# Kernel optimization log

Measured on AMD Instinct MI355X. Metric: run time of the kernel, lower is better.

Reference implementation:

```python
import jax, jax.numpy as jnp
import numpy as np

B, N = 64, 1024


def setup_inputs() -> dict:
    key = jax.random.key(0)
    k1, k2, k3, k4 = jax.random.split(key, 4)
    successor_logits = jax.random.normal(k1, (B, N, N), dtype=jnp.float32)
    predecessor_logits = jax.random.normal(k2, (B, N, N), dtype=jnp.float32)
    # labels in [-1, N); -1 means 'points to self'
    successor_labels = jax.random.randint(k3, (B, N), -1, N, dtype=jnp.int64)
    predecessor_labels = jax.random.randint(k4, (B, N), -1, N, dtype=jnp.int64)
    line_mask = jnp.ones((B, N), dtype=bool)
    return {
        "successor_logits": successor_logits,
        "successor_labels": successor_labels,
        "predecessor_logits": predecessor_logits,
        "predecessor_labels": predecessor_labels,
        "line_mask": line_mask,
        "pred_weight": jnp.float32(1.0),
    }


def _direction_loss(logits, labels, line_mask, is_self_pointing):
    b, n = labels.shape
    line_idx = jnp.arange(n)
    # relabel self-pointing lines to their own index
    labels_fixed = jnp.where(is_self_pointing, line_idx[None, :], labels)
    # overwrite diagonal logit with (row max + 1) where self-pointing & valid
    row_max = jnp.max(logits, axis=-1)  # [B, N]
    cond = is_self_pointing & line_mask  # [B, N]
    eye = jnp.eye(n, dtype=bool)
    logits_adj = jnp.where(cond[:, :, None] & eye[None], (row_max + 1.0)[:, :, None], logits)
    # softmax cross-entropy per line
    logp = jax.nn.log_softmax(logits_adj, axis=-1)  # [B, N, N]
    lbl = jnp.clip(labels_fixed, 0, n - 1)
    nll = -jnp.take_along_axis(logp, lbl[:, :, None], axis=-1)[..., 0]  # [B, N]
    valid = line_mask.astype(logits.dtype)
    denom = jnp.maximum(valid.sum(), 1.0)
    return (nll * valid).sum() / denom


def reference(successor_logits, successor_labels, predecessor_logits,
              predecessor_labels, line_mask, pred_weight):
    last_line_mask = successor_labels == -1
    succ_loss = _direction_loss(successor_logits, successor_labels, line_mask, last_line_mask)
    first_line_mask = predecessor_labels == -1
    pred_loss = _direction_loss(predecessor_logits, predecessor_labels, line_mask, first_line_mask)
    total_loss = succ_loss + pred_weight * pred_loss
    num_valid = line_mask.sum()
    return total_loss, succ_loss, pred_loss, num_valid
```

## Files before the change

kernel.cpp:

```cpp
#include <hip/hip_runtime.h>
#include <math.h>

#define N_ 1024
#define ROWS_PER_DIR 65536
#define TOTAL_ROWS   131072
#define BLOCKS_K1    32768

__global__ __launch_bounds__(256) void row_loss_kernel(
    const float* __restrict__ succ_logits,
    const int*   __restrict__ succ_labels,
    const float* __restrict__ pred_logits,
    const int*   __restrict__ pred_labels,
    const int*   __restrict__ line_mask,
    float*       __restrict__ partials)
{
    __shared__ float wsum[4];
    const int wave = threadIdx.x >> 6;
    const int lane = threadIdx.x & 63;
    const int r    = blockIdx.x * 4 + wave;
    const int dir  = r >> 16;
    const int rr   = r & (ROWS_PER_DIR - 1);
    const int n    = rr & (N_ - 1);

    const float* __restrict__ logits = dir ? pred_logits : succ_logits;
    const int*   __restrict__ labels = dir ? pred_labels : succ_labels;
    const float* __restrict__ row    = logits + (size_t)rr * N_;

    const float4* row4 = (const float4*)row;
    float4 v0 = row4[0 * 64 + lane];
    float4 v1 = row4[1 * 64 + lane];
    float4 v2 = row4[2 * 64 + lane];
    float4 v3 = row4[3 * 64 + lane];

    float m = v0.x;
    m = fmaxf(m, v0.y); m = fmaxf(m, v0.z); m = fmaxf(m, v0.w);
    m = fmaxf(m, v1.x); m = fmaxf(m, v1.y); m = fmaxf(m, v1.z); m = fmaxf(m, v1.w);
    m = fmaxf(m, v2.x); m = fmaxf(m, v2.y); m = fmaxf(m, v2.z); m = fmaxf(m, v2.w);
    m = fmaxf(m, v3.x); m = fmaxf(m, v3.y); m = fmaxf(m, v3.z); m = fmaxf(m, v3.w);

    float s = 0.0f;
    s += __expf(v0.x - m); s += __expf(v0.y - m); s += __expf(v0.z - m); s += __expf(v0.w - m);
    s += __expf(v1.x - m); s += __expf(v1.y - m); s += __expf(v1.z - m); s += __expf(v1.w - m);
    s += __expf(v2.x - m); s += __expf(v2.y - m); s += __expf(v2.z - m); s += __expf(v2.w - m);
    s += __expf(v3.x - m); s += __expf(v3.y - m); s += __expf(v3.z - m); s += __expf(v3.w - m);

    #pragma unroll
    for (int off = 32; off > 0; off >>= 1) {
        float mo = __shfl_xor(m, off);
        float so = __shfl_xor(s, off);
        float M  = fmaxf(m, mo);
        s = s * __expf(m - M) + so * __expf(mo - M);
        m = M;
    }

    if (lane == 0) {
        float nll_masked = 0.0f;
        const int label = labels[rr];
        const int valid = line_mask[rr];
        if (valid) {
            if (label == -1) {
                float d = row[n];
                float s_adj = (s - __expf(d - m)) * 0.36787944117144233f + 1.0f;
                nll_masked = __logf(s_adj);
            } else {
                int lbl = label < 0 ? 0 : (label > N_ - 1 ? N_ - 1 : label);
                nll_masked = m + __logf(s) - row[lbl];
            }
        }
        wsum[wave] = nll_masked;
    }
    __syncthreads();
    if (threadIdx.x == 0)
        partials[blockIdx.x] = (wsum[0] + wsum[1]) + (wsum[2] + wsum[3]);
}

__global__ __launch_bounds__(1024) void finalize_kernel(
    const float* __restrict__ partials,
    const int*   __restrict__ line_mask,
    const float* __restrict__ pred_weight,
    float*       __restrict__ out)
{
    const int tid = threadIdx.x;
    float ssum = 0.0f, psum = 0.0f, msum = 0.0f;
    for (int i = tid; i < BLOCKS_K1 / 2; i += 1024) {
        ssum += partials[i];
        psum += partials[i + BLOCKS_K1 / 2];
    }
    for (int i = tid; i < ROWS_PER_DIR; i += 1024)
        msum += (line_mask[i] != 0) ? 1.0f : 0.0f;

    #pragma unroll
    for (int off = 32; off > 0; off >>= 1) {
        ssum += __shfl_xor(ssum, off);
        psum += __shfl_xor(psum, off);
        msum += __shfl_xor(msum, off);
    }

    __shared__ float sh[3][16];
    const int wave = tid >> 6, lane = tid & 63;
    if (lane == 0) { sh[0][wave] = ssum; sh[1][wave] = psum; sh[2][wave] = msum; }
    __syncthreads();
    if (tid == 0) {
        float S = 0.0f, P = 0.0f, M = 0.0f;
        #pragma unroll
        for (int w = 0; w < 16; ++w) { S += sh[0][w]; P += sh[1][w]; M += sh[2][w]; }
        const float denom = fmaxf(M, 1.0f);
        const float sl = S / denom, pl = P / denom;
        const float w  = pred_weight[0];
        out[0] = sl + w * pl;
        out[1] = sl;
        out[2] = pl;
        out[3] = M;
    }
}

extern "C" void kernel_launch(void* const* d_in, const int* in_sizes, int n_in,
                              void* d_out, int out_size, void* d_ws, size_t ws_size,
                              hipStream_t stream) {
    const float* succ_logits = (const float*)d_in[0];
    const int*   succ_labels = (const int*)  d_in[1];
    const float* pred_logits = (const float*)d_in[2];
    const int*   pred_labels = (const int*)  d_in[3];
    const int*   line_mask   = (const int*)  d_in[4];
    const float* pred_weight = (const float*)d_in[5];
    float* out      = (float*)d_out;
    float* partials = (float*)d_ws;

    row_loss_kernel<<<BLOCKS_K1, 256, 0, stream>>>(
        succ_logits, succ_labels, pred_logits, pred_labels, line_mask, partials);
    finalize_kernel<<<1, 1024, 0, stream>>>(partials, line_mask, pred_weight, out);
}
```

Before: 523.9 us.

## Use nontemporal loads, two-pass wave reduction, and in-register target gather

Reads rows with nontemporal vector loads and raises the block to 8 waves. The max reduction now finishes across the wave before the exp pass, so the cross-lane sum reduction no longer needs rescaling exps. The target logit is taken from registers with a shuffle instead of a second global load, and label and mask are loaded early. The kernel is bound by memory bandwidth, so the main lever is how the streaming reads are cached. The shuffle-based gather adds a little ALU work.

```diff
diff --git a/kernel.cpp b/kernel.cpp
--- a/kernel.cpp
+++ b/kernel.cpp
@@ -4,9 +4,12 @@
 #define N_ 1024
 #define ROWS_PER_DIR 65536
 #define TOTAL_ROWS   131072
-#define BLOCKS_K1    32768
+#define WAVES_PER_BLOCK 8
+#define BLOCKS_K1    (TOTAL_ROWS / WAVES_PER_BLOCK)
 
-__global__ __launch_bounds__(256) void row_loss_kernel(
+typedef float v4f __attribute__((ext_vector_type(4)));
+
+__global__ __launch_bounds__(512) void row_loss_kernel(
     const float* __restrict__ succ_logits,
     const int*   __restrict__ succ_labels,
     const float* __restrict__ pred_logits,
@@ -14,10 +17,10 @@
     const int*   __restrict__ line_mask,
     float*       __restrict__ partials)
 {
-    __shared__ float wsum[4];
+    __shared__ float wsum[WAVES_PER_BLOCK];
     const int wave = threadIdx.x >> 6;
     const int lane = threadIdx.x & 63;
-    const int r    = blockIdx.x * 4 + wave;
+    const int r    = blockIdx.x * WAVES_PER_BLOCK + wave;
     const int dir  = r >> 16;
     const int rr   = r & (ROWS_PER_DIR - 1);
     const int n    = rr & (N_ - 1);
@@ -26,52 +29,62 @@
     const int*   __restrict__ labels = dir ? pred_labels : succ_labels;
     const float* __restrict__ row    = logits + (size_t)rr * N_;
 
-    const float4* row4 = (const float4*)row;
-    float4 v0 = row4[0 * 64 + lane];
-    float4 v1 = row4[1 * 64 + lane];
-    float4 v2 = row4[2 * 64 + lane];
-    float4 v3 = row4[3 * 64 + lane];
+    const int label = labels[rr];
+    const int valid = line_mask[rr];
 
-    float m = v0.x;
-    m = fmaxf(m, v0.y); m = fmaxf(m, v0.z); m = fmaxf(m, v0.w);
-    m = fmaxf(m, v1.x); m = fmaxf(m, v1.y); m = fmaxf(m, v1.z); m = fmaxf(m, v1.w);
-    m = fmaxf(m, v2.x); m = fmaxf(m, v2.y); m = fmaxf(m, v2.z); m = fmaxf(m, v2.w);
-    m = fmaxf(m, v3.x); m = fmaxf(m, v3.y); m = fmaxf(m, v3.z); m = fmaxf(m, v3.w);
+    const v4f* row4 = (const v4f*)row;
+    v4f v0 = __builtin_nontemporal_load(row4 + 0 * 64 + lane);
+    v4f v1 = __builtin_nontemporal_load(row4 + 1 * 64 + lane);
+    v4f v2 = __builtin_nontemporal_load(row4 + 2 * 64 + lane);
+    v4f v3 = __builtin_nontemporal_load(row4 + 3 * 64 + lane);
+
+    const int t      = (label == -1) ? n : (label < 0 ? 0 : (label > N_ - 1 ? N_ - 1 : label));
+    const int t_lane = (t >> 2) & 63;
+    const int t_k    = t >> 8;
+    const int t_c    = t & 3;
+    v4f tv = (t_k == 0) ? v0 : (t_k == 1) ? v1 : (t_k == 2) ? v2 : v3;
+    const float x_t = __shfl(tv[t_c], t_lane);
+
+    float m;
+    {
+        v4f a = v0, b = v1;
+        a.x = fmaxf(a.x, b.x); a.y = fmaxf(a.y, b.y); a.z = fmaxf(a.z, b.z); a.w = fmaxf(a.w, b.w);
+        v4f c = v2; b = v3;
+        c.x = fmaxf(c.x, b.x); c.y = fmaxf(c.y, b.y); c.z = fmaxf(c.z, b.z); c.w = fmaxf(c.w, b.w);
+        a.x = fmaxf(a.x, c.x); a.y = fmaxf(a.y, c.y); a.z = fmaxf(a.z, c.z); a.w = fmaxf(a.w, c.w);
+        m = fmaxf(fmaxf(a.x, a.y), fmaxf(a.z, a.w));
+    }
+    #pragma unroll
+    for (int off = 32; off > 0; off >>= 1)
+        m = fmaxf(m, __shfl_xor(m, off));
 
     float s = 0.0f;
     s += __expf(v0.x - m); s += __expf(v0.y - m); s += __expf(v0.z - m); s += __expf(v0.w - m);
     s += __expf(v1.x - m); s += __expf(v1.y - m); s += __expf(v1.z - m); s += __expf(v1.w - m);
     s += __expf(v2.x - m); s += __expf(v2.y - m); s += __expf(v2.z - m); s += __expf(v2.w - m);
     s += __expf(v3.x - m); s += __expf(v3.y - m); s += __expf(v3.z - m); s += __expf(v3.w - m);
-
     #pragma unroll
-    for (int off = 32; off > 0; off >>= 1) {
-        float mo = __shfl_xor(m, off);
-        float so = __shfl_xor(s, off);
-        float M  = fmaxf(m, mo);
-        s = s * __expf(m - M) + so * __expf(mo - M);
-        m = M;
-    }
+    for (int off = 32; off > 0; off >>= 1)
+        s += __shfl_xor(s, off);
 
     if (lane == 0) {
-        float nll_masked = 0.0f;
-        const int label = labels[rr];
-        const int valid = line_mask[rr];
+        float nll = 0.0f;
         if (valid) {
             if (label == -1) {
-                float d = row[n];
-                float s_adj = (s - __expf(d - m)) * 0.36787944117144233f + 1.0f;
-                nll_masked = __logf(s_adj);
+                nll = __logf((s - __expf(x_t - m)) * 0.36787944117144233f + 1.0f);
             } else {
-                int lbl = label < 0 ? 0 : (label > N_ - 1 ? N_ - 1 : label);
-                nll_masked = m + __logf(s) - row[lbl];
+                nll = m + __logf(s) - x_t;
             }
         }
-        wsum[wave] = nll_masked;
+        wsum[wave] = nll;
     }
     __syncthreads();
-    if (threadIdx.x == 0)
-        partials[blockIdx.x] = (wsum[0] + wsum[1]) + (wsum[2] + wsum[3]);
+    if (threadIdx.x == 0) {
+        float acc = 0.0f;
+        #pragma unroll
+        for (int w = 0; w < WAVES_PER_BLOCK; ++w) acc += wsum[w];
+        partials[blockIdx.x] = acc;
+    }
 }
 
 __global__ __launch_bounds__(1024) void finalize_kernel(
@@ -126,7 +139,7 @@
     float* out      = (float*)d_out;
     float* partials = (float*)d_ws;
 
-    row_loss_kernel<<<BLOCKS_K1, 256, 0, stream>>>(
+    row_loss_kernel<<<BLOCKS_K1, 512, 0, stream>>>(
         succ_logits, succ_labels, pred_logits, pred_labels, line_mask, partials);
     finalize_kernel<<<1, 1024, 0, stream>>>(partials, line_mask, pred_weight, out);
 }
```

New measurement: 494.3 us. 5.6% less time.
